# Kernel optimization log

Hardware: AMD Instinct MI355X
Metric: run time of the kernel (lower is better)

The kernel has to match this reference:

```python
import jax, jax.numpy as jnp
import numpy as np

N_FFT = 1024
HOP = 256
CACHE = N_FFT - 1  # causal left padding
EPS = 1e-12
BATCH = 16
SAMPLES = HOP * 2048


def _make_weight():
    # DFT basis modulated by a periodic Hann window (torch.hann_window default).
    n = np.arange(N_FFT, dtype=np.float32)
    k = np.arange(N_FFT // 2 + 1, dtype=np.float32)[:, None]
    ang = (-2.0 * np.pi / N_FFT) * k * n[None, :]
    win = 0.5 * (1.0 - np.cos(2.0 * np.pi * n / N_FFT))
    w = np.concatenate([np.cos(ang), np.sin(ang)], axis=0) * win  # [2*(N//2+1), N_FFT]
    return jnp.asarray(w, dtype=jnp.float32)[:, None, :]  # [O, I=1, K]


def setup_inputs() -> dict:
    key = jax.random.key(0)
    x = jax.random.normal(key, (BATCH, SAMPLES), dtype=jnp.float32)
    return {"x": x, "weight": _make_weight()}


def reference(x, weight):
    if x.ndim == 2:
        x = x[:, None, :]  # [B, 1, T]
    # causal constant (zero) padding on the left
    x = jnp.pad(x, ((0, 0), (0, 0), (CACHE, 0)))
    # strided conv against the fixed DFT basis: [B, 2*(N//2+1), L]
    y = jax.lax.conv_general_dilated(
        x, weight, window_strides=(HOP,), padding='VALID',
        dimension_numbers=('NCH', 'OIH', 'NCH'))
    B, C, T = y.shape
    y = y.reshape(B, 2, C // 2, T)  # real/imag split
    mag = jnp.sqrt(jnp.clip(jnp.sum(y * y, axis=1), EPS, None))  # [B, N//2+1, L]
    return mag
```

## Files before the change

### kernel.cpp

```cpp
#include <hip/hip_runtime.h>
#include <stdint.h>

#define SAMPLES   524288
#define BATCH     16
#define T_FRAMES  2048
#define K_FFT     1024
#define HOPSZ     256
#define CACHEPAD  1023
#define NCH       513
#define NCH_PAD   576
#define XROW      525312

typedef __bf16          bf16x8 __attribute__((ext_vector_type(8)));
typedef float           f32x4  __attribute__((ext_vector_type(4)));
typedef unsigned short  u16x8  __attribute__((ext_vector_type(8)));

__device__ __forceinline__ unsigned short f2bf(float f) {
    union { float f; unsigned u; } v; v.f = f;
    unsigned r = v.u + 0x7fffu + ((v.u >> 16) & 1u);
    return (unsigned short)(r >> 16);
}

__global__ void x2bf(const float* __restrict__ x, unsigned short* __restrict__ Xb) {
    int bat = blockIdx.y;
    unsigned short* xbo = Xb + (long long)bat * XROW;
    if (blockIdx.x == 0) {
        for (int j = threadIdx.x; j < CACHEPAD; j += 256) xbo[j] = 0;
        xbo[XROW - 1] = 0;
    }
    int i0 = (blockIdx.x * 256 + threadIdx.x) * 8;
    if (i0 >= SAMPLES) return;
    const float* xb = x + (long long)bat * SAMPLES;
    f32x4 a = *(const f32x4*)&xb[i0];
    f32x4 b = *(const f32x4*)&xb[i0 + 4];
    unsigned short* dst = xbo + CACHEPAD + i0;
    #pragma unroll
    for (int e = 0; e < 4; ++e) dst[e]     = f2bf(a[e]);
    #pragma unroll
    for (int e = 0; e < 4; ++e) dst[4 + e] = f2bf(b[e]);
}

__global__ void weight_prep(const float* __restrict__ w, unsigned short* __restrict__ Wb) {
    int i = blockIdx.x * blockDim.x + threadIdx.x;
    int k = i & 1023;
    int c = (i >> 10) % NCH_PAD;
    int s = i / (NCH_PAD * 1024);
    if (s >= 2) return;
    float v = (c < NCH) ? w[((long long)(s * NCH + c)) * K_FFT + k] : 0.f;
    Wb[i] = f2bf(v);
}

__device__ __forceinline__ void gll16(const unsigned short* g, unsigned short* s) {
    __builtin_amdgcn_global_load_lds(
        (const __attribute__((address_space(1))) void*)g,
        (__attribute__((address_space(3))) void*)s,
        16, 0, 0);
}

__global__ __launch_bounds__(256, 3)
void stft_gemm(const unsigned short* __restrict__ Xb,
               const unsigned short* __restrict__ Wb,
               float* __restrict__ out) {
    __shared__ unsigned short Ws[128 * 64];
    __shared__ unsigned short Fs[128 * 64];

    const int id  = blockIdx.x;
    const int xcd = id & 7;
    const int idx = id >> 3;
    const int nt  = idx >> 5;
    const int ft  = (xcd << 5) | (idx & 31);

    const int tid = threadIdx.x;
    const int l   = tid & 63;
    const int w   = tid >> 6;
    const int ln  = l & 15;
    const int qd  = l >> 4;

    const int b  = ft >> 4;
    const int t0 = (ft & 15) * 128;

    const unsigned short* xbase = Xb + (long long)b * XROW;

    const int srow   = l >> 3;
    const int schunk = l & 7;

    const unsigned short* fsrc[4];
    const unsigned short* wsrc[4];
    unsigned short* fdst[4];
    unsigned short* wdst[4];
    #pragma unroll
    for (int c = 0; c < 4; ++c) {
        int r = w * 32 + c * 8 + srow;
        int gchunk = schunk ^ (r & 7);
        fsrc[c] = xbase + (t0 + r) * HOPSZ + gchunk * 8;
        int sel = (r >> 4) & 1;
        int chl = ((r >> 5) << 4) | (r & 15);
        int ch  = nt * 64 + chl;
        wsrc[c] = Wb + ((long long)(sel * NCH_PAD + ch)) * K_FFT + gchunk * 8;
        fdst[c] = Fs + (w * 32 + c * 8) * 64;
        wdst[c] = Ws + (w * 32 + c * 8) * 64;
    }

    const int wave_m = w & 1;
    const int wave_n = w >> 1;

    f32x4 acc[4][4];
    #pragma unroll
    for (int i = 0; i < 4; ++i)
        #pragma unroll
        for (int j = 0; j < 4; ++j)
            acc[i][j] = (f32x4){0.f, 0.f, 0.f, 0.f};

    int a_off[4][2], b_off[4][2];
    #pragma unroll
    for (int i = 0; i < 4; ++i)
        #pragma unroll
        for (int k2 = 0; k2 < 2; ++k2) {
            int ck = ((k2 * 4 + qd) ^ (ln & 7)) * 8;
            a_off[i][k2] = (wave_m * 64 + i * 16 + ln) * 64 + ck;
            b_off[i][k2] = (wave_n * 64 + i * 16 + ln) * 64 + ck;
        }

    for (int kk = 0; kk < K_FFT; kk += 64) {
        #pragma unroll
        for (int c = 0; c < 4; ++c) gll16(fsrc[c] + kk, fdst[c]);
        #pragma unroll
        for (int c = 0; c < 4; ++c) gll16(wsrc[c] + kk, wdst[c]);
        __syncthreads();

        #pragma unroll
        for (int k2 = 0; k2 < 2; ++k2) {
            bf16x8 av[4], bv[4];
            #pragma unroll
            for (int i = 0; i < 4; ++i) av[i] = *(const bf16x8*)&Ws[a_off[i][k2]];
            #pragma unroll
            for (int j = 0; j < 4; ++j) bv[j] = *(const bf16x8*)&Fs[b_off[j][k2]];
            #pragma unroll
            for (int i = 0; i < 4; ++i)
                #pragma unroll
                for (int j = 0; j < 4; ++j)
                    acc[i][j] = __builtin_amdgcn_mfma_f32_16x16x32_bf16(av[i], bv[j], acc[i][j], 0, 0, 0);
        }
        __syncthreads();
    }

    #pragma unroll
    for (int p = 0; p < 2; ++p) {
        #pragma unroll
        for (int j = 0; j < 4; ++j) {
            #pragma unroll
            for (int r = 0; r < 4; ++r) {
                float re  = acc[2 * p][j][r];
                float im  = acc[2 * p + 1][j][r];
                float mag = sqrtf(fmaxf(re * re + im * im, 1e-12f));
                int ch = nt * 64 + (wave_m * 2 + p) * 16 + qd * 4 + r;
                int t  = t0 + wave_n * 64 + j * 16 + ln;
                if (ch < NCH)
                    out[((long long)b * NCH + ch) * T_FRAMES + t] = mag;
            }
        }
    }
}

extern "C" void kernel_launch(void* const* d_in, const int* in_sizes, int n_in,
                              void* d_out, int out_size, void* d_ws, size_t ws_size,
                              hipStream_t stream) {
    const float* x  = (const float*)d_in[0];
    const float* wt = (const float*)d_in[1];
    float* out = (float*)d_out;

    unsigned short* Xb = (unsigned short*)d_ws;
    unsigned short* Wb = (unsigned short*)((char*)d_ws + (size_t)33554432);

    dim3 xgrid(SAMPLES / (256 * 8), 16);
    x2bf<<<xgrid, 256, 0, stream>>>(x, Xb);
    weight_prep<<<4608, 256, 0, stream>>>(wt, Wb);
    stft_gemm<<<dim3(2304), 256, 0, stream>>>(Xb, Wb, out);
}
```

Baseline: 166.1 us.

## Enlarge GEMM tiles, pipeline LDS loads, fold Nyquist bin into DC imag slot, merge prep kernels

The two prep kernels become one launch. The weight is repacked into 512 rows by placing the Nyquist bin in the unused imaginary slot of bin 0, which removes the padding to 576 channels and the wasted MFMA work on padded rows. The GEMM now uses 512-thread blocks with 256x256 tiles. A double-buffered, prefetch-ahead schedule uses global_load_lds, explicit vmcnt waits, split barriers and setprio so loads overlap MFMA work. The larger tiles and 128KB of LDS cut occupancy to one block of 8 waves per CU, and the grid drops to 512 blocks, which may cause wave-quantization effects on 256 CUs.

Result: faster. 154.3 us (-7.1%).

```diff
diff --git a/kernel.cpp b/kernel.cpp
--- a/kernel.cpp
+++ b/kernel.cpp
@@ -8,7 +8,6 @@
 #define HOPSZ     256
 #define CACHEPAD  1023
 #define NCH       513
-#define NCH_PAD   576
 #define XROW      525312
 
 typedef __bf16          bf16x8 __attribute__((ext_vector_type(8)));
@@ -21,33 +20,41 @@
     return (unsigned short)(r >> 16);
 }
 
-__global__ void x2bf(const float* __restrict__ x, unsigned short* __restrict__ Xb) {
-    int bat = blockIdx.y;
-    unsigned short* xbo = Xb + (long long)bat * XROW;
-    if (blockIdx.x == 0) {
-        for (int j = threadIdx.x; j < CACHEPAD; j += 256) xbo[j] = 0;
-        xbo[XROW - 1] = 0;
+__global__ void prep(const float* __restrict__ x, const float* __restrict__ wsrc,
+                     unsigned short* __restrict__ Xb, unsigned short* __restrict__ Wb) {
+    const int bid = blockIdx.x;
+    const int tid = threadIdx.x;
+    if (bid < 512) {
+        int gid = bid * 256 + tid;
+        int m   = gid >> 7;
+        int kc  = (gid & 127) << 3;
+        int q = m >> 5, h = (m >> 4) & 1, r = m & 15;
+        int bin  = q * 16 + r;
+        int srow = (h == 0) ? bin : (bin == 0 ? 512 : NCH + bin);
+        const float* s = wsrc + (long long)srow * K_FFT + kc;
+        f32x4 a = *(const f32x4*)s;
+        f32x4 c = *(const f32x4*)(s + 4);
+        union { u16x8 v; unsigned short e[8]; } o;
+        o.e[0]=f2bf(a[0]); o.e[1]=f2bf(a[1]); o.e[2]=f2bf(a[2]); o.e[3]=f2bf(a[3]);
+        o.e[4]=f2bf(c[0]); o.e[5]=f2bf(c[1]); o.e[6]=f2bf(c[2]); o.e[7]=f2bf(c[3]);
+        *(u16x8*)(Wb + (long long)m * K_FFT + kc) = o.v;
+    } else {
+        int id  = bid - 512;
+        int bat = id >> 8;
+        int bx  = id & 255;
+        unsigned short* xbo = Xb + (long long)bat * XROW;
+        if (bx == 0) {
+            for (int j = tid; j < CACHEPAD; j += 256) xbo[j] = 0;
+            if (tid == 0) xbo[XROW - 1] = 0;
+        }
+        int i0 = (bx * 256 + tid) * 8;
+        const float* xb = x + (long long)bat * SAMPLES;
+        f32x4 a = *(const f32x4*)&xb[i0];
+        f32x4 c = *(const f32x4*)&xb[i0 + 4];
+        unsigned short* dst = xbo + CACHEPAD + i0;
+        dst[0]=f2bf(a[0]); dst[1]=f2bf(a[1]); dst[2]=f2bf(a[2]); dst[3]=f2bf(a[3]);
+        dst[4]=f2bf(c[0]); dst[5]=f2bf(c[1]); dst[6]=f2bf(c[2]); dst[7]=f2bf(c[3]);
     }
-    int i0 = (blockIdx.x * 256 + threadIdx.x) * 8;
-    if (i0 >= SAMPLES) return;
-    const float* xb = x + (long long)bat * SAMPLES;
-    f32x4 a = *(const f32x4*)&xb[i0];
-    f32x4 b = *(const f32x4*)&xb[i0 + 4];
-    unsigned short* dst = xbo + CACHEPAD + i0;
-    #pragma unroll
-    for (int e = 0; e < 4; ++e) dst[e]     = f2bf(a[e]);
-    #pragma unroll
-    for (int e = 0; e < 4; ++e) dst[4 + e] = f2bf(b[e]);
-}
-
-__global__ void weight_prep(const float* __restrict__ w, unsigned short* __restrict__ Wb) {
-    int i = blockIdx.x * blockDim.x + threadIdx.x;
-    int k = i & 1023;
-    int c = (i >> 10) % NCH_PAD;
-    int s = i / (NCH_PAD * 1024);
-    if (s >= 2) return;
-    float v = (c < NCH) ? w[((long long)(s * NCH + c)) * K_FFT + k] : 0.f;
-    Wb[i] = f2bf(v);
 }
 
 __device__ __forceinline__ void gll16(const unsigned short* g, unsigned short* s) {
@@ -57,106 +64,162 @@
         16, 0, 0);
 }
 
-__global__ __launch_bounds__(256, 3)
+#define MFMA(a,b,c) __builtin_amdgcn_mfma_f32_16x16x32_bf16((a),(b),(c),0,0,0)
+
+__global__ __launch_bounds__(512, 2)
 void stft_gemm(const unsigned short* __restrict__ Xb,
                const unsigned short* __restrict__ Wb,
                float* __restrict__ out) {
-    __shared__ unsigned short Ws[128 * 64];
-    __shared__ unsigned short Fs[128 * 64];
+    __shared__ unsigned short S[65536];
 
     const int id  = blockIdx.x;
     const int xcd = id & 7;
-    const int idx = id >> 3;
-    const int nt  = idx >> 5;
-    const int ft  = (xcd << 5) | (idx & 31);
+    const int u   = id >> 3;
+    const int nt  = u >> 4;
+    const int ft  = (xcd << 4) | (u & 15);
+    const int b   = ft >> 3;
+    const int t0  = (ft & 7) << 8;
 
     const int tid = threadIdx.x;
     const int l   = tid & 63;
-    const int w   = tid >> 6;
+    const int wv  = tid >> 6;
     const int ln  = l & 15;
     const int qd  = l >> 4;
-
-    const int b  = ft >> 4;
-    const int t0 = (ft & 15) * 128;
-
+    const int wm  = wv & 1;
+    const int wn  = wv >> 1;
+
+    const int sr0 = wv * 32 + (l >> 2);
+    const int sr1 = sr0 + 16;
+    const int sch = ((l & 3) ^ ((l >> 3) & 3)) * 8;
+    const unsigned short* wA0 = Wb + (long long)(nt * 256 + sr0) * K_FFT + sch;
+    const unsigned short* wA1 = Wb + (long long)(nt * 256 + sr1) * K_FFT + sch;
     const unsigned short* xbase = Xb + (long long)b * XROW;
-
-    const int srow   = l >> 3;
-    const int schunk = l & 7;
-
-    const unsigned short* fsrc[4];
-    const unsigned short* wsrc[4];
-    unsigned short* fdst[4];
-    unsigned short* wdst[4];
+    const unsigned short* fB0 = xbase + (t0 + sr0) * HOPSZ + sch;
+    const unsigned short* fB1 = xbase + (t0 + sr1) * HOPSZ + sch;
+    const int d0 = wv * 1024;
+    const int d1 = d0 + 512;
+
+    const int cx   = (qd ^ ((ln >> 1) & 3)) * 8;
+    const int aoff = (wm * 128 + ln) * 32 + cx;
+    const int boff = (wn * 64  + ln) * 32 + cx;
+
+    f32x4 acc[8][4];
     #pragma unroll
-    for (int c = 0; c < 4; ++c) {
-        int r = w * 32 + c * 8 + srow;
-        int gchunk = schunk ^ (r & 7);
-        fsrc[c] = xbase + (t0 + r) * HOPSZ + gchunk * 8;
-        int sel = (r >> 4) & 1;
-        int chl = ((r >> 5) << 4) | (r & 15);
-        int ch  = nt * 64 + chl;
-        wsrc[c] = Wb + ((long long)(sel * NCH_PAD + ch)) * K_FFT + gchunk * 8;
-        fdst[c] = Fs + (w * 32 + c * 8) * 64;
-        wdst[c] = Ws + (w * 32 + c * 8) * 64;
+    for (int i = 0; i < 8; ++i)
+        #pragma unroll
+        for (int jn = 0; jn < 4; ++jn) acc[i][jn] = (f32x4){0.f,0.f,0.f,0.f};
+
+    gll16(wA0 +  0, S +     0 + d0);  gll16(wA1 +  0, S +     0 + d1);
+    gll16(fB0 +  0, S +  8192 + d0);  gll16(fB1 +  0, S +  8192 + d1);
+    gll16(wA0 + 32, S + 16384 + d0);  gll16(wA1 + 32, S + 16384 + d1);
+    gll16(fB0 + 32, S + 24576 + d0);  gll16(fB1 + 32, S + 24576 + d1);
+    gll16(wA0 + 64, S + 32768 + d0);  gll16(wA1 + 64, S + 32768 + d1);
+    gll16(fB0 + 64, S + 40960 + d0);  gll16(fB1 + 64, S + 40960 + d1);
+    asm volatile("s_waitcnt vmcnt(4)" ::: "memory");
+    __builtin_amdgcn_s_barrier();
+
+    #pragma unroll 1
+    for (int j = 0; j < 16; ++j) {
+        const int bb  = (j & 1) << 15;
+        const int bb1 = bb ^ 32768;
+        const int kA  = j * 64 + 96;
+        const int kB  = j * 64 + 128;
+
+        bf16x8 av[8];
+        if (j < 15) { gll16(wA0 + kA, S + bb1 + 16384 + d0);
+                      gll16(wA1 + kA, S + bb1 + 16384 + d1); }
+        {
+            const unsigned short* pA = S + bb + aoff;
+            const unsigned short* pB = S + bb + 8192 + boff;
+            #pragma unroll
+            for (int i = 0; i < 8; ++i) av[i] = *(const bf16x8*)(pA + i * 512);
+            bf16x8 b0 = *(const bf16x8*)(pB);
+            bf16x8 b1 = *(const bf16x8*)(pB + 512);
+            __builtin_amdgcn_s_barrier();
+            __builtin_amdgcn_s_setprio(1);
+            #pragma unroll
+            for (int i = 0; i < 8; ++i) {
+                acc[i][0] = MFMA(av[i], b0, acc[i][0]);
+                acc[i][1] = MFMA(av[i], b1, acc[i][1]);
+            }
+            __builtin_amdgcn_s_setprio(0);
+            __builtin_amdgcn_s_barrier();
+        }
+        if (j < 15) { gll16(fB0 + kA, S + bb1 + 24576 + d0);
+                      gll16(fB1 + kA, S + bb1 + 24576 + d1); }
+        {
+            const unsigned short* pB = S + bb + 8192 + boff;
+            bf16x8 b2 = *(const bf16x8*)(pB + 1024);
+            bf16x8 b3 = *(const bf16x8*)(pB + 1536);
+            __builtin_amdgcn_s_barrier();
+            __builtin_amdgcn_s_setprio(1);
+            #pragma unroll
+            for (int i = 0; i < 8; ++i) {
+                acc[i][2] = MFMA(av[i], b2, acc[i][2]);
+                acc[i][3] = MFMA(av[i], b3, acc[i][3]);
+            }
+            __builtin_amdgcn_s_setprio(0);
+            __builtin_amdgcn_s_barrier();
+        }
+        if (j < 14) { gll16(wA0 + kB, S + bb + d0);
+                      gll16(wA1 + kB, S + bb + d1); }
+        {
+            const unsigned short* pA = S + bb + 16384 + aoff;
+            const unsigned short* pB = S + bb + 24576 + boff;
+            #pragma unroll
+            for (int i = 0; i < 8; ++i) av[i] = *(const bf16x8*)(pA + i * 512);
+            bf16x8 b0 = *(const bf16x8*)(pB);
+            bf16x8 b1 = *(const bf16x8*)(pB + 512);
+            __builtin_amdgcn_s_barrier();
+            __builtin_amdgcn_s_setprio(1);
+            #pragma unroll
+            for (int i = 0; i < 8; ++i) {
+                acc[i][0] = MFMA(av[i], b0, acc[i][0]);
+                acc[i][1] = MFMA(av[i], b1, acc[i][1]);
+            }
+            __builtin_amdgcn_s_setprio(0);
+            __builtin_amdgcn_s_barrier();
+        }
+        if (j < 14) { gll16(fB0 + kB, S + bb + 8192 + d0);
+                      gll16(fB1 + kB, S + bb + 8192 + d1); }
+        {
+            const unsigned short* pB = S + bb + 24576 + boff;
+            bf16x8 b2 = *(const bf16x8*)(pB + 1024);
+            bf16x8 b3 = *(const bf16x8*)(pB + 1536);
+            __builtin_amdgcn_s_barrier();
+            __builtin_amdgcn_s_setprio(1);
+            #pragma unroll
+            for (int i = 0; i < 8; ++i) {
+                acc[i][2] = MFMA(av[i], b2, acc[i][2]);
+                acc[i][3] = MFMA(av[i], b3, acc[i][3]);
+            }
+            __builtin_amdgcn_s_setprio(0);
+            if (j == 14) { asm volatile("s_waitcnt vmcnt(0)" ::: "memory"); }
+            else         { asm volatile("s_waitcnt vmcnt(4)" ::: "memory"); }
+            __builtin_amdgcn_s_barrier();
+        }
     }
 
-    const int wave_m = w & 1;
-    const int wave_n = w >> 1;
-
-    f32x4 acc[4][4];
+    float* outb = out + (long long)b * (NCH * T_FRAMES);
+    const int tb = t0 + wn * 64 + ln;
+    const int binbase = (nt * 8 + wm * 4) * 16 + qd * 4;
     #pragma unroll
-    for (int i = 0; i < 4; ++i)
+    for (int p = 0; p < 4; ++p) {
         #pragma unroll
-        for (int j = 0; j < 4; ++j)
-            acc[i][j] = (f32x4){0.f, 0.f, 0.f, 0.f};
-
-    int a_off[4][2], b_off[4][2];
-    #pragma unroll
-    for (int i = 0; i < 4; ++i)
-        #pragma unroll
-        for (int k2 = 0; k2 < 2; ++k2) {
-            int ck = ((k2 * 4 + qd) ^ (ln & 7)) * 8;
-            a_off[i][k2] = (wave_m * 64 + i * 16 + ln) * 64 + ck;
-            b_off[i][k2] = (wave_n * 64 + i * 16 + ln) * 64 + ck;
-        }
-
-    for (int kk = 0; kk < K_FFT; kk += 64) {
-        #pragma unroll
-        for (int c = 0; c < 4; ++c) gll16(fsrc[c] + kk, fdst[c]);
-        #pragma unroll
-        for (int c = 0; c < 4; ++c) gll16(wsrc[c] + kk, wdst[c]);
-        __syncthreads();
-
-        #pragma unroll
-        for (int k2 = 0; k2 < 2; ++k2) {
-            bf16x8 av[4], bv[4];
-            #pragma unroll
-            for (int i = 0; i < 4; ++i) av[i] = *(const bf16x8*)&Ws[a_off[i][k2]];
-            #pragma unroll
-            for (int j = 0; j < 4; ++j) bv[j] = *(const bf16x8*)&Fs[b_off[j][k2]];
-            #pragma unroll
-            for (int i = 0; i < 4; ++i)
-                #pragma unroll
-                for (int j = 0; j < 4; ++j)
-                    acc[i][j] = __builtin_amdgcn_mfma_f32_16x16x32_bf16(av[i], bv[j], acc[i][j], 0, 0, 0);
-        }
-        __syncthreads();
-    }
-
-    #pragma unroll
-    for (int p = 0; p < 2; ++p) {
-        #pragma unroll
-        for (int j = 0; j < 4; ++j) {
+        for (int jn = 0; jn < 4; ++jn) {
+            const int t = tb + jn * 16;
             #pragma unroll
             for (int r = 0; r < 4; ++r) {
-                float re  = acc[2 * p][j][r];
-                float im  = acc[2 * p + 1][j][r];
-                float mag = sqrtf(fmaxf(re * re + im * im, 1e-12f));
-                int ch = nt * 64 + (wave_m * 2 + p) * 16 + qd * 4 + r;
-                int t  = t0 + wave_n * 64 + j * 16 + ln;
-                if (ch < NCH)
-                    out[((long long)b * NCH + ch) * T_FRAMES + t] = mag;
+                float re = acc[2 * p][jn][r];
+                float im = acc[2 * p + 1][jn][r];
+                int bin = binbase + p * 16 + r;
+                if (bin == 0) {
+                    outb[t] = sqrtf(fmaxf(re * re, 1e-12f));
+                    outb[(long long)512 * T_FRAMES + t] = sqrtf(fmaxf(im * im, 1e-12f));
+                } else {
+                    outb[(long long)bin * T_FRAMES + t] =
+                        sqrtf(fmaxf(re * re + im * im, 1e-12f));
+                }
             }
         }
     }
@@ -172,8 +235,6 @@
     unsigned short* Xb = (unsigned short*)d_ws;
     unsigned short* Wb = (unsigned short*)((char*)d_ws + (size_t)33554432);
 
-    dim3 xgrid(SAMPLES / (256 * 8), 16);
-    x2bf<<<xgrid, 256, 0, stream>>>(x, Xb);
-    weight_prep<<<4608, 256, 0, stream>>>(wt, Wb);
-    stft_gemm<<<dim3(2304), 256, 0, stream>>>(Xb, Wb, out);
-}
+    prep<<<4608, 256, 0, stream>>>(x, wt, Xb, Wb);
+    stft_gemm<<<512, 512, 0, stream>>>(Xb, Wb, out);
+}
```

## Pack Nyquist bin into DC slot to cut channel tiles, fuse prep kernels

Applied to the files above, without the earlier changes.

Uses the fact that the DC bin's imaginary part is zero and the Nyquist bin's imaginary part is zero. The Nyquist real row goes into the DC imaginary slot, so 512 packed channels cover all 513 bins. This removes the ninth channel tile (2304 to 2048 GEMM blocks) and the zero padding in the weight buffer. The two prep kernels are also merged into one vectorized launch. The risk is that the packing relies on the basis rows being exactly zero for those imaginary parts.

Result: faster. 154.1 us (-7.2%).

```diff
diff --git a/kernel.cpp b/kernel.cpp
--- a/kernel.cpp
+++ b/kernel.cpp
@@ -8,7 +8,6 @@
 #define HOPSZ     256
 #define CACHEPAD  1023
 #define NCH       513
-#define NCH_PAD   576
 #define XROW      525312
 
 typedef __bf16          bf16x8 __attribute__((ext_vector_type(8)));
@@ -21,33 +20,41 @@
     return (unsigned short)(r >> 16);
 }
 
-__global__ void x2bf(const float* __restrict__ x, unsigned short* __restrict__ Xb) {
-    int bat = blockIdx.y;
-    unsigned short* xbo = Xb + (long long)bat * XROW;
-    if (blockIdx.x == 0) {
-        for (int j = threadIdx.x; j < CACHEPAD; j += 256) xbo[j] = 0;
-        xbo[XROW - 1] = 0;
+__global__ void prep(const float* __restrict__ x, const float* __restrict__ wsrc,
+                     unsigned short* __restrict__ Xb, unsigned short* __restrict__ Wb) {
+    const int bid = blockIdx.x;
+    const int tid = threadIdx.x;
+    if (bid < 512) {
+        int gid = bid * 256 + tid;
+        int m   = gid >> 7;
+        int kc  = (gid & 127) << 3;
+        int q = m >> 5, h = (m >> 4) & 1, r = m & 15;
+        int bin  = q * 16 + r;
+        int srow = (h == 0) ? bin : (bin == 0 ? 512 : NCH + bin);
+        const float* s = wsrc + (long long)srow * K_FFT + kc;
+        f32x4 a = *(const f32x4*)s;
+        f32x4 c = *(const f32x4*)(s + 4);
+        union { u16x8 v; unsigned short e[8]; } o;
+        o.e[0]=f2bf(a[0]); o.e[1]=f2bf(a[1]); o.e[2]=f2bf(a[2]); o.e[3]=f2bf(a[3]);
+        o.e[4]=f2bf(c[0]); o.e[5]=f2bf(c[1]); o.e[6]=f2bf(c[2]); o.e[7]=f2bf(c[3]);
+        *(u16x8*)(Wb + (long long)m * K_FFT + kc) = o.v;
+    } else {
+        int id  = bid - 512;
+        int bat = id >> 8;
+        int bx  = id & 255;
+        unsigned short* xbo = Xb + (long long)bat * XROW;
+        if (bx == 0) {
+            for (int j = tid; j < CACHEPAD; j += 256) xbo[j] = 0;
+            if (tid == 0) xbo[XROW - 1] = 0;
+        }
+        int i0 = (bx * 256 + tid) * 8;
+        const float* xb = x + (long long)bat * SAMPLES;
+        f32x4 a = *(const f32x4*)&xb[i0];
+        f32x4 c = *(const f32x4*)&xb[i0 + 4];
+        unsigned short* dst = xbo + CACHEPAD + i0;
+        dst[0]=f2bf(a[0]); dst[1]=f2bf(a[1]); dst[2]=f2bf(a[2]); dst[3]=f2bf(a[3]);
+        dst[4]=f2bf(c[0]); dst[5]=f2bf(c[1]); dst[6]=f2bf(c[2]); dst[7]=f2bf(c[3]);
     }
-    int i0 = (blockIdx.x * 256 + threadIdx.x) * 8;
-    if (i0 >= SAMPLES) return;
-    const float* xb = x + (long long)bat * SAMPLES;
-    f32x4 a = *(const f32x4*)&xb[i0];
-    f32x4 b = *(const f32x4*)&xb[i0 + 4];
-    unsigned short* dst = xbo + CACHEPAD + i0;
-    #pragma unroll
-    for (int e = 0; e < 4; ++e) dst[e]     = f2bf(a[e]);
-    #pragma unroll
-    for (int e = 0; e < 4; ++e) dst[4 + e] = f2bf(b[e]);
-}
-
-__global__ void weight_prep(const float* __restrict__ w, unsigned short* __restrict__ Wb) {
-    int i = blockIdx.x * blockDim.x + threadIdx.x;
-    int k = i & 1023;
-    int c = (i >> 10) % NCH_PAD;
-    int s = i / (NCH_PAD * 1024);
-    if (s >= 2) return;
-    float v = (c < NCH) ? w[((long long)(s * NCH + c)) * K_FFT + k] : 0.f;
-    Wb[i] = f2bf(v);
 }
 
 __device__ __forceinline__ void gll16(const unsigned short* g, unsigned short* s) {
@@ -93,10 +100,7 @@
         int r = w * 32 + c * 8 + srow;
         int gchunk = schunk ^ (r & 7);
         fsrc[c] = xbase + (t0 + r) * HOPSZ + gchunk * 8;
-        int sel = (r >> 4) & 1;
-        int chl = ((r >> 5) << 4) | (r & 15);
-        int ch  = nt * 64 + chl;
-        wsrc[c] = Wb + ((long long)(sel * NCH_PAD + ch)) * K_FFT + gchunk * 8;
+        wsrc[c] = Wb + ((long long)(nt * 128 + r)) * K_FFT + gchunk * 8;
         fdst[c] = Fs + (w * 32 + c * 8) * 64;
         wdst[c] = Ws + (w * 32 + c * 8) * 64;
     }
@@ -144,19 +148,24 @@
         __syncthreads();
     }
 
+    float* outb = out + (long long)b * (NCH * T_FRAMES);
     #pragma unroll
     for (int p = 0; p < 2; ++p) {
         #pragma unroll
         for (int j = 0; j < 4; ++j) {
+            const int t = t0 + wave_n * 64 + j * 16 + ln;
             #pragma unroll
             for (int r = 0; r < 4; ++r) {
                 float re  = acc[2 * p][j][r];
                 float im  = acc[2 * p + 1][j][r];
-                float mag = sqrtf(fmaxf(re * re + im * im, 1e-12f));
-                int ch = nt * 64 + (wave_m * 2 + p) * 16 + qd * 4 + r;
-                int t  = t0 + wave_n * 64 + j * 16 + ln;
-                if (ch < NCH)
-                    out[((long long)b * NCH + ch) * T_FRAMES + t] = mag;
+                int bin = (nt * 4 + wave_m * 2 + p) * 16 + qd * 4 + r;
+                if (bin == 0) {
+                    outb[t] = sqrtf(fmaxf(re * re, 1e-12f));
+                    outb[(long long)512 * T_FRAMES + t] = sqrtf(fmaxf(im * im, 1e-12f));
+                } else {
+                    outb[(long long)bin * T_FRAMES + t] =
+                        sqrtf(fmaxf(re * re + im * im, 1e-12f));
+                }
             }
         }
     }
@@ -172,8 +181,6 @@
     unsigned short* Xb = (unsigned short*)d_ws;
     unsigned short* Wb = (unsigned short*)((char*)d_ws + (size_t)33554432);
 
-    dim3 xgrid(SAMPLES / (256 * 8), 16);
-    x2bf<<<xgrid, 256, 0, stream>>>(x, Xb);
-    weight_prep<<<4608, 256, 0, stream>>>(wt, Wb);
-    stft_gemm<<<dim3(2304), 256, 0, stream>>>(Xb, Wb, out);
+    prep<<<4608, 256, 0, stream>>>(x, wt, Xb, Wb);
+    stft_gemm<<<2048, 256, 0, stream>>>(Xb, Wb, out);
 }
```
